# Optimization experiments

Hardware: AMD Instinct MI355X
Metric: run time of the kernel (lower is better)

## Reference

```python
import jax, jax.numpy as jnp
import numpy as np

B, P, K, HE, HF = 256, 128, 512, 1024, 512
D = K + HE + 2 * HF  # 2560, MLP input dim
HID = 64


def setup_inputs() -> dict:
    key = jax.random.key(0)
    ks = jax.random.split(key, 6)
    query = jax.random.normal(ks[0], (B, 1, HE), dtype=jnp.float32)
    keys = jax.random.normal(ks[1], (B, P, K), dtype=jnp.float32)
    frameLSTM_h = jax.random.normal(ks[2], (B, 1, 2 * HF), dtype=jnp.float32)
    mask = jax.random.randint(ks[3], (B, P), 0, 2, dtype=jnp.int32)
    mask = mask.at[:, 0].set(1)  # guarantee at least one unmasked player per row
    W1 = jax.random.normal(ks[4], (D, HID), dtype=jnp.float32) / np.float32(np.sqrt(D))
    W2 = jax.random.normal(ks[5], (HID, 1), dtype=jnp.float32) / np.float32(np.sqrt(HID))
    return dict(query=query, keys=keys, frameLSTM_h=frameLSTM_h, mask=mask, W1=W1, W2=W2)


def reference(query, keys, frameLSTM_h, mask, W1, W2):
    # Faithful to: cat([keys, query.repeat, frame.repeat]) @ W1 -> ReLU -> @ W2.
    # The pre-activation is linear, so splitting W1 by row-blocks is exactly the
    # same math without materializing the repeated/concatenated (B,P,D) tensor.
    W1k = W1[:K]            # (K, 64)
    W1q = W1[K:K + HE]      # (HE, 64)
    W1f = W1[K + HE:]       # (2*HF, 64)
    h = jax.nn.relu(
        jnp.einsum('bpk,kh->bph', keys, W1k)
        + jnp.einsum('boe,eh->boh', query, W1q)        # broadcasts over P
        + jnp.einsum('bof,fh->boh', frameLSTM_h, W1f)  # broadcasts over P
    )  # (B, P, 64)
    raw_scores = jnp.einsum('bph,ho->bp', h, W2)  # (B, P)
    raw_scores = jnp.where(mask == 0, -jnp.inf, raw_scores)
    weights = jax.nn.softmax(raw_scores, axis=1)  # (B, P)
    context = jnp.einsum('bp,bpk->bk', weights, keys)[:, None, :]  # (B, 1, K)
    embeddings = jnp.concatenate([context, frameLSTM_h], axis=2)   # (B, 1, K+2*HF)
    return embeddings, weights
```

## Files before the change

kernel.cpp:

```cpp
#include <hip/hip_runtime.h>
#include <hip/hip_bf16.h>
#include <cstdint>
#include <math.h>


typedef __bf16 bf16;
typedef __attribute__((ext_vector_type(8))) __bf16 bf16x8;
typedef __attribute__((ext_vector_type(4))) __bf16 bf16x4;
typedef __attribute__((ext_vector_type(4))) float f32x4;

#define NB 256
#define NP 128
#define NK 512
#define SKLD 520
#define SK_BYTES (NP * SKLD * 2)
#define SQF_OFF  SK_BYTES
#define SCORES_OFF (SQF_OFF + 4096)
#define WTS_OFF    (SCORES_OFF + 512)
#define PP_OFF     (WTS_OFF + 512)
#define W2_OFF     (PP_OFF + 2048)
#define CP_OFF     (W2_OFF + 256)
#define SMEM_BYTES (CP_OFF + 2048)

__global__ __launch_bounds__(256) void prep_kernel(
    const float* __restrict__ W1, bf16* __restrict__ w1kt,
    bf16* __restrict__ w1qft)
{
    const int blk = blockIdx.x;
    const int t = threadIdx.x;
    __shared__ float s[32][65];
    if (blk < 16) {
        const int k0 = blk * 32;
#pragma unroll
        for (int i = 0; i < 8; i++) {
            const int idx = t + 256 * i;
            const int k = idx >> 6, h = idx & 63;
            s[k][h] = W1[(size_t)(k0 + k) * 64 + h];
        }
        __syncthreads();
#pragma unroll
        for (int i = 0; i < 8; i++) {
            const int idx = t + 256 * i;
            const int h = idx >> 5, kk = idx & 31;
            w1kt[(size_t)h * 512 + k0 + kk] = (bf16)s[kk][h];
        }
    } else {
        const int j = blk - 16;
        const int d0 = j * 32;
#pragma unroll
        for (int i = 0; i < 8; i++) {
            const int idx = t + 256 * i;
            const int r = idx >> 6, h = idx & 63;
            s[r][h] = W1[(size_t)(512 + d0 + r) * 64 + h];
        }
        __syncthreads();
#pragma unroll
        for (int i = 0; i < 8; i++) {
            const int idx = t + 256 * i;
            const int h = idx >> 5, rr = idx & 31;
            w1qft[(size_t)h * 2048 + d0 + rr] = (bf16)s[rr][h];
        }
    }
}

__global__ __launch_bounds__(512, 2) void attn_kernel(
    const float* __restrict__ keys, const float* __restrict__ query,
    const float* __restrict__ frame, const int* __restrict__ mask,
    const float* __restrict__ W2, const bf16* __restrict__ w1kt,
    const bf16* __restrict__ w1qft, float* __restrict__ out)
{
    extern __shared__ char smem[];
    bf16* sk      = (bf16*)smem;
    bf16* sqf     = (bf16*)(smem + SQF_OFF);
    float* scores = (float*)(smem + SCORES_OFF);
    float* wts    = (float*)(smem + WTS_OFF);
    float* pp     = (float*)(smem + PP_OFF);
    float* w2l    = (float*)(smem + W2_OFF);
    float* cpart  = (float*)(smem + CP_OFF);

    const int b = blockIdx.x;
    const int t = threadIdx.x;
    const int w = t >> 6;
    const int lane = t & 63;
    const int m = lane & 15;
    const int q = lane >> 4;

    if (t < 64) w2l[t] = W2[t];

    {
        const float* qsrc = (t < 256 ? query : frame) + (size_t)b * 1024 + (t & 255) * 4;
        const float4 qv = *(const float4*)qsrc;

        const int rowadd = t >> 7;
        const int c0 = (t & 127) * 4;
        const float* kb = keys + (size_t)b * (NP * NK);
        float4 kv[2][8];
#pragma unroll
        for (int ii = 0; ii < 8; ii++)
            kv[0][ii] = *(const float4*)(kb + (size_t)(4 * ii + rowadd) * 512 + (t & 127) * 4);

        bf16x4 qb;
        qb[0] = (bf16)qv.x; qb[1] = (bf16)qv.y; qb[2] = (bf16)qv.z; qb[3] = (bf16)qv.w;
        *(bf16x4*)(sqf + t * 4) = qb;

#pragma unroll
        for (int g = 0; g < 4; g++) {
            const int cur = g & 1;
            if (g < 3) {
#pragma unroll
                for (int ii = 0; ii < 8; ii++)
                    kv[cur ^ 1][ii] = *(const float4*)(
                        kb + (size_t)(4 * ((g + 1) * 8 + ii) + rowadd) * 512 + (t & 127) * 4);
            }
#pragma unroll
            for (int ii = 0; ii < 8; ii++) {
                const float4 v = kv[cur][ii];
                bf16x4 bv;
                bv[0] = (bf16)v.x; bv[1] = (bf16)v.y;
                bv[2] = (bf16)v.z; bv[3] = (bf16)v.w;
                *(bf16x4*)(sk + (size_t)(4 * (g * 8 + ii) + rowadd) * SKLD + c0) = bv;
            }
        }
    }
    __syncthreads();

    {
        const bf16* wb = w1qft + (size_t)m * 2048 + w * 256 + q * 8;
        f32x4 pacc[4];
#pragma unroll
        for (int nt = 0; nt < 4; nt++) pacc[nt] = (f32x4){0.f, 0.f, 0.f, 0.f};

        bf16x8 Bp[4];
#pragma unroll
        for (int nt = 0; nt < 4; nt++) Bp[nt] = *(const bf16x8*)(wb + nt * 32768);

#pragma unroll
        for (int kk = 0; kk < 8; kk++) {
            const bf16x8 Af = *(const bf16x8*)(sqf + w * 256 + kk * 32 + q * 8);
            bf16x8 Bc[4];
#pragma unroll
            for (int nt = 0; nt < 4; nt++) Bc[nt] = Bp[nt];
            if (kk < 7) {
#pragma unroll
                for (int nt = 0; nt < 4; nt++)
                    Bp[nt] = *(const bf16x8*)(wb + nt * 32768 + (kk + 1) * 32);
            }
#pragma unroll
            for (int nt = 0; nt < 4; nt++)
                pacc[nt] = __builtin_amdgcn_mfma_f32_16x16x32_bf16(Af, Bc[nt], pacc[nt], 0, 0, 0);
        }
        if (q == 0) {
#pragma unroll
            for (int nt = 0; nt < 4; nt++)
                pp[w * 64 + nt * 16 + m] = pacc[nt][0];
        }
    }
    __syncthreads();

    const int pw = w * 16;
    bf16x8 Av[16];
#pragma unroll
    for (int kk = 0; kk < 16; kk++)
        Av[kk] = *(const bf16x8*)(sk + (pw + m) * SKLD + kk * 32 + q * 8);

    const bf16* bbase = w1kt + (size_t)m * 512 + q * 8;
    bf16x8 Bv[2][16];
#pragma unroll
    for (int kk = 0; kk < 16; kk++)
        Bv[0][kk] = *(const bf16x8*)(bbase + kk * 32);

    float pr[4] = {0.f, 0.f, 0.f, 0.f};
#pragma unroll
    for (int nt = 0; nt < 4; nt++) {
        const int cur = nt & 1;
        if (nt < 3) {
#pragma unroll
            for (int kk = 0; kk < 16; kk++)
                Bv[cur ^ 1][kk] = *(const bf16x8*)(bbase + (nt + 1) * 8192 + kk * 32);
        }
        f32x4 acc = (f32x4){0.f, 0.f, 0.f, 0.f};
#pragma unroll
        for (int kk = 0; kk < 16; kk++)
            acc = __builtin_amdgcn_mfma_f32_16x16x32_bf16(Av[kk], Bv[cur][kk], acc, 0, 0, 0);
        const int h = nt * 16 + m;
        const float pv = pp[h] + pp[64 + h] + pp[128 + h] + pp[192 + h]
                       + pp[256 + h] + pp[320 + h] + pp[384 + h] + pp[448 + h];
        const float wv = w2l[h];
#pragma unroll
        for (int r = 0; r < 4; r++)
            pr[r] += fmaxf(acc[r] + pv, 0.f) * wv;
    }

#pragma unroll
    for (int off = 1; off < 16; off <<= 1) {
#pragma unroll
        for (int r = 0; r < 4; r++) pr[r] += __shfl_xor(pr[r], off);
    }
    if (m == 0) {
        const int pbase = pw + q * 4;
#pragma unroll
        for (int r = 0; r < 4; r++) scores[pbase + r] = pr[r];
    }
    __syncthreads();

    if (w == 0) {
        const int pa = lane, pb = lane + 64;
        float s0 = (mask[b * 128 + pa] == 0) ? -INFINITY : scores[pa];
        float s1 = (mask[b * 128 + pb] == 0) ? -INFINITY : scores[pb];
        float mx = fmaxf(s0, s1);
#pragma unroll
        for (int off = 32; off; off >>= 1) mx = fmaxf(mx, __shfl_xor(mx, off));
        float e0 = __expf(s0 - mx), e1 = __expf(s1 - mx);
        float sum = e0 + e1;
#pragma unroll
        for (int off = 32; off; off >>= 1) sum += __shfl_xor(sum, off);
        const float inv = 1.0f / sum;
        e0 *= inv; e1 *= inv;
        wts[pa] = e0; wts[pb] = e1;
        float* wout = out + (size_t)NB * 1536;
        wout[b * 128 + pa] = e0;
        wout[b * 128 + pb] = e1;
    }
    __syncthreads();

    {
        const int tg = t >> 8;
        const int tc = t & 255;
        float a0 = 0.f, a1 = 0.f;
#pragma unroll 8
        for (int i = 0; i < 64; i++) {
            const int p = tg * 64 + i;
            const float wv = wts[p];
            const uint32_t uv = *(const uint32_t*)(sk + (size_t)p * SKLD + 2 * tc);
            a0 += wv * __uint_as_float(uv << 16);
            a1 += wv * __uint_as_float(uv & 0xffff0000u);
        }
        if (tg == 1) {
            cpart[2 * tc] = a0;
            cpart[2 * tc + 1] = a1;
        }
        __syncthreads();
        if (tg == 0) {
            out[(size_t)b * 1536 + 2 * tc]     = a0 + cpart[2 * tc];
            out[(size_t)b * 1536 + 2 * tc + 1] = a1 + cpart[2 * tc + 1];
        }
    }
    {
        const float2 fv = *(const float2*)(frame + (size_t)b * 1024 + t * 2);
        *(float2*)(out + (size_t)b * 1536 + 512 + t * 2) = fv;
    }
}

extern "C" void kernel_launch(void* const* d_in, const int* in_sizes, int n_in,
                              void* d_out, int out_size, void* d_ws, size_t ws_size,
                              hipStream_t stream) {
    const float* query = (const float*)d_in[0];
    const float* keys  = (const float*)d_in[1];
    const float* frame = (const float*)d_in[2];
    const int*   mask  = (const int*)d_in[3];
    const float* W1    = (const float*)d_in[4];
    const float* W2    = (const float*)d_in[5];
    float* out = (float*)d_out;

    bf16* w1kt  = (bf16*)d_ws;
    bf16* w1qft = (bf16*)((char*)d_ws + (64 << 10));

    hipFuncSetAttribute((const void*)attn_kernel,
                        hipFuncAttributeMaxDynamicSharedMemorySize, SMEM_BYTES);

    prep_kernel<<<80, 256, 0, stream>>>(W1, w1kt, w1qft);
    attn_kernel<<<256, 512, SMEM_BYTES, stream>>>(keys, query, frame, mask, W2,
                                                  w1kt, w1qft, out);
}
```

Measured before the change: 129.7 us.

## Stream keys through a 4-deep async global-to-LDS ring buffer in fp32

Replaces the up-front load of all 128 key rows, converted to bf16 in LDS, with async global_load_lds copies of 16-row fp32 chunks into a 4-slot ring. Each chunk is converted to bf16 at MFMA time, and each wave now computes one hidden-unit tile rather than one row tile. The context sum reuses the 64 rows still in the ring and re-fetches the first 64 rows through a second pipelined pass. This overlaps key loading with the score MFMAs and shrinks the LDS footprint. The cost is extra global/L2 reads for the context pass, idle waves 4-7 during score compute, and hand-tuned vmcnt waits.

Result: no change. 132.2 us (+2.0%).

```diff
diff --git a/kernel.cpp b/kernel.cpp
--- a/kernel.cpp
+++ b/kernel.cpp
@@ -12,15 +12,21 @@
 #define NB 256
 #define NP 128
 #define NK 512
-#define SKLD 520
-#define SK_BYTES (NP * SKLD * 2)
-#define SQF_OFF  SK_BYTES
-#define SCORES_OFF (SQF_OFF + 4096)
-#define WTS_OFF    (SCORES_OFF + 512)
-#define PP_OFF     (WTS_OFF + 512)
-#define W2_OFF     (PP_OFF + 2048)
-#define CP_OFF     (W2_OFF + 256)
-#define SMEM_BYTES (CP_OFF + 2048)
+#define RSTR 516
+#define CHUNK_F (16 * RSTR)
+#define BUF_BYTES (4 * CHUNK_F * 4)
+#define SQF_OFF   BUF_BYTES
+#define PP_OFF    (SQF_OFF + 4096)
+#define PRP_OFF   (PP_OFF + 2048)
+#define WTS_OFF   (PRP_OFF + 2048)
+#define W2_OFF    (WTS_OFF + 512)
+#define SMEM_BYTES (W2_OFF + 256)
+
+__device__ __forceinline__ void async_copy16(const float* g, float* l) {
+    __builtin_amdgcn_global_load_lds(
+        (const __attribute__((address_space(1))) void*)g,
+        (__attribute__((address_space(3))) void*)l, 16, 0, 0);
+}
 
 __global__ __launch_bounds__(256) void prep_kernel(
     const float* __restrict__ W1, bf16* __restrict__ w1kt,
@@ -70,13 +76,12 @@
     const bf16* __restrict__ w1qft, float* __restrict__ out)
 {
     extern __shared__ char smem[];
-    bf16* sk      = (bf16*)smem;
-    bf16* sqf     = (bf16*)(smem + SQF_OFF);
-    float* scores = (float*)(smem + SCORES_OFF);
+    float* buf    = (float*)smem;
+    bf16*  sqf    = (bf16*)(smem + SQF_OFF);
+    float* pp     = (float*)(smem + PP_OFF);
+    float* prp    = (float*)(smem + PRP_OFF);
     float* wts    = (float*)(smem + WTS_OFF);
-    float* pp     = (float*)(smem + PP_OFF);
     float* w2l    = (float*)(smem + W2_OFF);
-    float* cpart  = (float*)(smem + CP_OFF);
 
     const int b = blockIdx.x;
     const int t = threadIdx.x;
@@ -90,37 +95,9 @@
     {
         const float* qsrc = (t < 256 ? query : frame) + (size_t)b * 1024 + (t & 255) * 4;
         const float4 qv = *(const float4*)qsrc;
-
-        const int rowadd = t >> 7;
-        const int c0 = (t & 127) * 4;
-        const float* kb = keys + (size_t)b * (NP * NK);
-        float4 kv[2][8];
-#pragma unroll
-        for (int ii = 0; ii < 8; ii++)
-            kv[0][ii] = *(const float4*)(kb + (size_t)(4 * ii + rowadd) * 512 + (t & 127) * 4);
-
         bf16x4 qb;
         qb[0] = (bf16)qv.x; qb[1] = (bf16)qv.y; qb[2] = (bf16)qv.z; qb[3] = (bf16)qv.w;
         *(bf16x4*)(sqf + t * 4) = qb;
-
-#pragma unroll
-        for (int g = 0; g < 4; g++) {
-            const int cur = g & 1;
-            if (g < 3) {
-#pragma unroll
-                for (int ii = 0; ii < 8; ii++)
-                    kv[cur ^ 1][ii] = *(const float4*)(
-                        kb + (size_t)(4 * ((g + 1) * 8 + ii) + rowadd) * 512 + (t & 127) * 4);
-            }
-#pragma unroll
-            for (int ii = 0; ii < 8; ii++) {
-                const float4 v = kv[cur][ii];
-                bf16x4 bv;
-                bv[0] = (bf16)v.x; bv[1] = (bf16)v.y;
-                bv[2] = (bf16)v.z; bv[3] = (bf16)v.w;
-                *(bf16x4*)(sk + (size_t)(4 * (g * 8 + ii) + rowadd) * SKLD + c0) = bv;
-            }
-        }
     }
     __syncthreads();
 
@@ -129,11 +106,9 @@
         f32x4 pacc[4];
 #pragma unroll
         for (int nt = 0; nt < 4; nt++) pacc[nt] = (f32x4){0.f, 0.f, 0.f, 0.f};
-
         bf16x8 Bp[4];
 #pragma unroll
         for (int nt = 0; nt < 4; nt++) Bp[nt] = *(const bf16x8*)(wb + nt * 32768);
-
 #pragma unroll
         for (int kk = 0; kk < 8; kk++) {
             const bf16x8 Af = *(const bf16x8*)(sqf + w * 256 + kk * 32 + q * 8);
@@ -157,56 +132,80 @@
     }
     __syncthreads();
 
-    const int pw = w * 16;
-    bf16x8 Av[16];
+    const int nt = w & 3;
+    const int h = nt * 16 + m;
+    const float pv = pp[h] + pp[64 + h] + pp[128 + h] + pp[192 + h]
+                   + pp[256 + h] + pp[320 + h] + pp[384 + h] + pp[448 + h];
+    const float w2v = w2l[h];
+
+    bf16x8 Bv[16];
 #pragma unroll
     for (int kk = 0; kk < 16; kk++)
-        Av[kk] = *(const bf16x8*)(sk + (pw + m) * SKLD + kk * 32 + q * 8);
-
-    const bf16* bbase = w1kt + (size_t)m * 512 + q * 8;
-    bf16x8 Bv[2][16];
-#pragma unroll
-    for (int kk = 0; kk < 16; kk++)
-        Bv[0][kk] = *(const bf16x8*)(bbase + kk * 32);
-
-    float pr[4] = {0.f, 0.f, 0.f, 0.f};
-#pragma unroll
-    for (int nt = 0; nt < 4; nt++) {
-        const int cur = nt & 1;
-        if (nt < 3) {
-#pragma unroll
-            for (int kk = 0; kk < 16; kk++)
-                Bv[cur ^ 1][kk] = *(const bf16x8*)(bbase + (nt + 1) * 8192 + kk * 32);
-        }
+        Bv[kk] = *(const bf16x8*)(w1kt + (size_t)(nt * 16 + m) * 512 + kk * 32 + q * 8);
+
+    const float* kb = keys + (size_t)b * (NP * NK);
+
+    auto issue_chunk = [&](int c) {
+        const int cb = c & 3;
+#pragma unroll
+        for (int i = 0; i < 2; i++) {
+            const int rl = 2 * w + i;
+#pragma unroll
+            for (int hh = 0; hh < 2; hh++)
+                async_copy16(kb + (size_t)(16 * c + rl) * 512 + hh * 256 + lane * 4,
+                             buf + (size_t)cb * CHUNK_F + rl * RSTR + hh * 256);
+        }
+    };
+
+    auto compute_chunk = [&](int c) {
+        const float* ab = buf + (size_t)(c & 3) * CHUNK_F + m * RSTR + q * 8;
         f32x4 acc = (f32x4){0.f, 0.f, 0.f, 0.f};
 #pragma unroll
-        for (int kk = 0; kk < 16; kk++)
-            acc = __builtin_amdgcn_mfma_f32_16x16x32_bf16(Av[kk], Bv[cur][kk], acc, 0, 0, 0);
-        const int h = nt * 16 + m;
-        const float pv = pp[h] + pp[64 + h] + pp[128 + h] + pp[192 + h]
-                       + pp[256 + h] + pp[320 + h] + pp[384 + h] + pp[448 + h];
-        const float wv = w2l[h];
-#pragma unroll
-        for (int r = 0; r < 4; r++)
-            pr[r] += fmaxf(acc[r] + pv, 0.f) * wv;
-    }
-
-#pragma unroll
-    for (int off = 1; off < 16; off <<= 1) {
-#pragma unroll
-        for (int r = 0; r < 4; r++) pr[r] += __shfl_xor(pr[r], off);
-    }
-    if (m == 0) {
-        const int pbase = pw + q * 4;
-#pragma unroll
-        for (int r = 0; r < 4; r++) scores[pbase + r] = pr[r];
-    }
+        for (int kk = 0; kk < 16; kk++) {
+            const float4 fa = *(const float4*)(ab + kk * 32);
+            const float4 fb = *(const float4*)(ab + kk * 32 + 4);
+            bf16x8 Af;
+            Af[0] = (bf16)fa.x; Af[1] = (bf16)fa.y; Af[2] = (bf16)fa.z; Af[3] = (bf16)fa.w;
+            Af[4] = (bf16)fb.x; Af[5] = (bf16)fb.y; Af[6] = (bf16)fb.z; Af[7] = (bf16)fb.w;
+            acc = __builtin_amdgcn_mfma_f32_16x16x32_bf16(Af, Bv[kk], acc, 0, 0, 0);
+        }
+        float pr[4];
+#pragma unroll
+        for (int r = 0; r < 4; r++) pr[r] = fmaxf(acc[r] + pv, 0.f) * w2v;
+#pragma unroll
+        for (int off = 1; off < 16; off <<= 1) {
+#pragma unroll
+            for (int r = 0; r < 4; r++) pr[r] += __shfl_xor(pr[r], off);
+        }
+        if (m == 0) {
+#pragma unroll
+            for (int r = 0; r < 4; r++)
+                prp[nt * 128 + 16 * c + q * 4 + r] = pr[r];
+        }
+    };
+
+    issue_chunk(0); issue_chunk(1); issue_chunk(2);
+#define STEP(c, WSTR) \
+    asm volatile(WSTR "\ns_barrier" ::: "memory"); \
+    if ((c) + 3 < 8) issue_chunk((c) + 3); \
+    if (w < 4) compute_chunk(c);
+    STEP(0, "s_waitcnt vmcnt(8)")
+    STEP(1, "s_waitcnt vmcnt(8)")
+    STEP(2, "s_waitcnt vmcnt(8)")
+    STEP(3, "s_waitcnt vmcnt(8)")
+    STEP(4, "s_waitcnt vmcnt(8)")
+    STEP(5, "s_waitcnt vmcnt(8)")
+    STEP(6, "s_waitcnt vmcnt(4)")
+    STEP(7, "s_waitcnt vmcnt(0)")
+#undef STEP
     __syncthreads();
 
     if (w == 0) {
         const int pa = lane, pb = lane + 64;
-        float s0 = (mask[b * 128 + pa] == 0) ? -INFINITY : scores[pa];
-        float s1 = (mask[b * 128 + pb] == 0) ? -INFINITY : scores[pb];
+        float s0 = prp[pa] + prp[128 + pa] + prp[256 + pa] + prp[384 + pa];
+        float s1 = prp[pb] + prp[128 + pb] + prp[256 + pb] + prp[384 + pb];
+        s0 = (mask[b * 128 + pa] == 0) ? -INFINITY : s0;
+        s1 = (mask[b * 128 + pb] == 0) ? -INFINITY : s1;
         float mx = fmaxf(s0, s1);
 #pragma unroll
         for (int off = 32; off; off >>= 1) mx = fmaxf(mx, __shfl_xor(mx, off));
@@ -223,28 +222,33 @@
     }
     __syncthreads();
 
-    {
-        const int tg = t >> 8;
-        const int tc = t & 255;
-        float a0 = 0.f, a1 = 0.f;
-#pragma unroll 8
-        for (int i = 0; i < 64; i++) {
-            const int p = tg * 64 + i;
-            const float wv = wts[p];
-            const uint32_t uv = *(const uint32_t*)(sk + (size_t)p * SKLD + 2 * tc);
-            a0 += wv * __uint_as_float(uv << 16);
-            a1 += wv * __uint_as_float(uv & 0xffff0000u);
-        }
-        if (tg == 1) {
-            cpart[2 * tc] = a0;
-            cpart[2 * tc + 1] = a1;
-        }
-        __syncthreads();
-        if (tg == 0) {
-            out[(size_t)b * 1536 + 2 * tc]     = a0 + cpart[2 * tc];
-            out[(size_t)b * 1536 + 2 * tc + 1] = a1 + cpart[2 * tc + 1];
-        }
-    }
+    float ca = 0.f, cb2 = 0.f;
+#pragma unroll
+    for (int bi = 0; bi < 4; bi++) {
+#pragma unroll
+        for (int i = 0; i < 16; i += 2) {
+            ca  += wts[64 + bi * 16 + i]     * buf[(size_t)bi * CHUNK_F + i * RSTR + t];
+            cb2 += wts[64 + bi * 16 + i + 1] * buf[(size_t)bi * CHUNK_F + (i + 1) * RSTR + t];
+        }
+    }
+    __syncthreads();
+
+    issue_chunk(0); issue_chunk(1); issue_chunk(2);
+#define CSTEP(j, WSTR) \
+    asm volatile(WSTR "\ns_barrier" ::: "memory"); \
+    if ((j) + 3 < 4) issue_chunk((j) + 3); \
+    _Pragma("unroll") \
+    for (int i = 0; i < 16; i += 2) { \
+        ca  += wts[(j) * 16 + i]     * buf[(size_t)((j) & 3) * CHUNK_F + i * RSTR + t]; \
+        cb2 += wts[(j) * 16 + i + 1] * buf[(size_t)((j) & 3) * CHUNK_F + (i + 1) * RSTR + t]; \
+    }
+    CSTEP(0, "s_waitcnt vmcnt(8)")
+    CSTEP(1, "s_waitcnt vmcnt(8)")
+    CSTEP(2, "s_waitcnt vmcnt(4)")
+    CSTEP(3, "s_waitcnt vmcnt(0)")
+#undef CSTEP
+    out[(size_t)b * 1536 + t] = ca + cb2;
+
     {
         const float2 fv = *(const float2*)(frame + (size_t)b * 1024 + t * 2);
         *(float2*)(out + (size_t)b * 1536 + 512 + t * 2) = fv;
```
